# Performance work log

Hardware: AMD Instinct MI355X
Metric: run time of the kernel (lower is better)

## Reference

```python
import jax, jax.numpy as jnp
import numpy as np

N_HEAD = 8
HIDDEN = 512
HEAD_DIM = HIDDEN // N_HEAD
EPS = 1e-5


def _layernorm(x, g, b):
    mu = jnp.mean(x, axis=-1, keepdims=True)
    var = jnp.var(x, axis=-1, keepdims=True)
    return (x - mu) * jax.lax.rsqrt(var + EPS) * g + b


def setup_inputs() -> dict:
    key = jax.random.key(0)
    ks = jax.random.split(key, 12)
    s = 1.0 / np.sqrt(HIDDEN)
    x = jax.random.normal(ks[0], (4, 2048, HIDDEN), dtype=jnp.float32)
    # per-head Q/K/V projections stacked: [H, D, dh] weights, [H, dh] biases
    Wq = jax.random.uniform(ks[1], (N_HEAD, HIDDEN, HEAD_DIM), minval=-s, maxval=s, dtype=jnp.float32)
    bq = jax.random.uniform(ks[2], (N_HEAD, HEAD_DIM), minval=-s, maxval=s, dtype=jnp.float32)
    Wk = jax.random.uniform(ks[3], (N_HEAD, HIDDEN, HEAD_DIM), minval=-s, maxval=s, dtype=jnp.float32)
    bk = jax.random.uniform(ks[4], (N_HEAD, HEAD_DIM), minval=-s, maxval=s, dtype=jnp.float32)
    Wv = jax.random.uniform(ks[5], (N_HEAD, HIDDEN, HEAD_DIM), minval=-s, maxval=s, dtype=jnp.float32)
    bv = jax.random.uniform(ks[6], (N_HEAD, HEAD_DIM), minval=-s, maxval=s, dtype=jnp.float32)
    Wm = jax.random.uniform(ks[7], (HIDDEN, HIDDEN), minval=-s, maxval=s, dtype=jnp.float32)
    bm = jax.random.uniform(ks[8], (HIDDEN,), minval=-s, maxval=s, dtype=jnp.float32)
    Wo = jax.random.uniform(ks[9], (HIDDEN, HIDDEN), minval=-s, maxval=s, dtype=jnp.float32)
    bo = jax.random.uniform(ks[10], (HIDDEN,), minval=-s, maxval=s, dtype=jnp.float32)
    g1 = jnp.ones((HIDDEN,), jnp.float32); b1 = jnp.zeros((HIDDEN,), jnp.float32)
    g2 = jnp.ones((HIDDEN,), jnp.float32); b2 = jnp.zeros((HIDDEN,), jnp.float32)
    return {"x": x, "g1": g1, "b1": b1, "Wq": Wq, "bq": bq, "Wk": Wk, "bk": bk,
            "Wv": Wv, "bv": bv, "Wm": Wm, "bm": bm, "g2": g2, "b2": b2, "Wo": Wo, "bo": bo}


def reference(x, g1, b1, Wq, bq, Wk, bk, Wv, bv, Wm, bm, g2, b2, Wo, bo):
    h = _layernorm(x, g1, b1)                                 # [B,S,D]
    # stacked per-head projections: [B,H,S,dh]
    q = jnp.einsum('bsd,hde->bhse', h, Wq) + bq[None, :, None, :]
    k = jnp.einsum('bsd,hde->bhse', h, Wk) + bk[None, :, None, :]
    v = jnp.einsum('bsd,hde->bhse', h, Wv) + bv[None, :, None, :]
    scores = jnp.einsum('bhse,bhte->bhst', q, k) / jnp.sqrt(jnp.float32(HEAD_DIM))
    attn = jax.nn.softmax(scores, axis=-1)                    # [B,H,S,S]
    out = jnp.einsum('bhst,bhte->bhse', attn, v)              # [B,H,S,dh]
    B, H, S, E = out.shape
    out_mha = jnp.transpose(out, (0, 2, 1, 3)).reshape(B, S, H * E)  # concat heads
    h_ln_post = out_mha @ Wm + bm + x
    h_fc = _layernorm(h_ln_post, g2, b2)
    return jax.nn.relu(h_fc @ Wo + bo) + h_ln_post
```

## Files before the change

### kernel.cpp

```cpp
#include <hip/hip_runtime.h>
#include <hip/hip_bf16.h>


typedef __attribute__((ext_vector_type(8))) short bf16x8;
typedef __attribute__((ext_vector_type(4))) float f32x4;
typedef __attribute__((ext_vector_type(16))) float f32x16;
typedef __attribute__((ext_vector_type(8))) unsigned short u16x8;

typedef union { bf16x8 v; unsigned u[4]; u16x8 s; } frag_u;

typedef const unsigned int __attribute__((address_space(1)))* gas_t;
typedef unsigned int __attribute__((address_space(3)))* las_t;
static __device__ __forceinline__ void glds16(const void* g, void* l) {
    __builtin_amdgcn_global_load_lds((gas_t)g, (las_t)l, 16, 0, 0);
}

static __device__ __forceinline__ unsigned short f2b(float f) {
    union { float f; unsigned u; } a; a.f = f;
    unsigned r = a.u + 0x7FFFu + ((a.u >> 16) & 1u);
    return (unsigned short)(r >> 16);
}
static __device__ __forceinline__ float b2f(unsigned short u) {
    union { unsigned u; float f; } c; c.u = ((unsigned)u) << 16; return c.f;
}
static __device__ __forceinline__ unsigned pack_bf16(float lo, float hi) {
    __hip_bfloat162 p = __float22bfloat162_rn(make_float2(lo, hi));
    unsigned r; __builtin_memcpy(&r, &p, 4); return r;
}
static __device__ __forceinline__ float fexp2(float x) {
#if __has_builtin(__builtin_amdgcn_exp2f)
    return __builtin_amdgcn_exp2f(x);
#else
    return exp2f(x);
#endif
}
static __device__ __forceinline__ void swap32(int hi, unsigned a, unsigned b,
                                              unsigned& x, unsigned& y) {
#if __has_builtin(__builtin_amdgcn_permlane32_swap)
    typedef __attribute__((ext_vector_type(2))) int i32x2;
    i32x2 r = __builtin_amdgcn_permlane32_swap((int)a, (int)b, false, false);
    x = (unsigned)r[0]; y = (unsigned)r[1];
#else
    unsigned ta = (unsigned)__shfl_xor((int)a, 32);
    unsigned tb = (unsigned)__shfl_xor((int)b, 32);
    x = hi ? tb : a;
    y = hi ? b : ta;
#endif
}

static __device__ __forceinline__ void ln_row(
    const float* __restrict__ X, const float* __restrict__ gam,
    const float* __restrict__ bet, unsigned short* __restrict__ O,
    int row, int lane)
{
    const float4* xr = (const float4*)(X + (size_t)row * 512);
    float4 v0 = xr[lane * 2], v1 = xr[lane * 2 + 1];
    float vv[8] = {v0.x, v0.y, v0.z, v0.w, v1.x, v1.y, v1.z, v1.w};
    float s = 0.f, s2 = 0.f;
    #pragma unroll
    for (int j = 0; j < 8; ++j) { s += vv[j]; s2 += vv[j] * vv[j]; }
    #pragma unroll
    for (int d = 1; d < 64; d <<= 1) { s += __shfl_xor(s, d); s2 += __shfl_xor(s2, d); }
    float mean = s * (1.0f / 512.0f);
    float var  = s2 * (1.0f / 512.0f) - mean * mean;
    float rstd = rsqrtf(var + 1e-5f);
    int c = lane * 8;
    u16x8 o;
    #pragma unroll
    for (int j = 0; j < 8; ++j) o[j] = f2b((vv[j] - mean) * rstd * gam[c + j] + bet[c + j]);
    *(u16x8*)(O + (size_t)row * 512 + c) = o;
}

__global__ __launch_bounds__(256) void prep_ln_k(
    const float* __restrict__ Wq, const float* __restrict__ Wk, const float* __restrict__ Wv,
    const float* __restrict__ Wm, const float* __restrict__ Wo,
    unsigned short* __restrict__ wqT, unsigned short* __restrict__ wkT,
    unsigned short* __restrict__ wvT, unsigned short* __restrict__ wmT,
    unsigned short* __restrict__ woT,
    const float* __restrict__ X, const float* __restrict__ g1,
    const float* __restrict__ b1, unsigned short* __restrict__ h1)
{
    int bx = blockIdx.x;
    if (bx < 1024) {
        int idx = bx * 256 + threadIdx.x;
        int n = idx >> 9, k = idx & 511;
        int h = n >> 6, e = n & 63;
        size_t src_qkv = ((size_t)h * 512 + k) * 64 + e;
        wqT[idx] = f2b(Wq[src_qkv]);
        wkT[idx] = f2b(Wk[src_qkv]);
        wvT[idx] = f2b(Wv[src_qkv]);
        wmT[idx] = f2b(Wm[(size_t)k * 512 + n]);
        woT[idx] = f2b(Wo[(size_t)k * 512 + n]);
    } else {
        int row = (bx - 1024) * 4 + (threadIdx.x >> 6);
        ln_row(X, g1, b1, h1, row, threadIdx.x & 63);
    }
}

__global__ __launch_bounds__(256) void ln4_k(
    const float* __restrict__ X, const float* __restrict__ gam,
    const float* __restrict__ bet, unsigned short* __restrict__ O)
{
    int row = blockIdx.x * 4 + (threadIdx.x >> 6);
    ln_row(X, gam, bet, O, row, threadIdx.x & 63);
}

__global__ __launch_bounds__(256) void gemm_qkv_k(
    const unsigned short* __restrict__ A, const unsigned short* __restrict__ Bt,
    const float* __restrict__ bq, const float* __restrict__ bk, const float* __restrict__ bv,
    unsigned short* __restrict__ Qo, unsigned short* __restrict__ Ko,
    unsigned short* __restrict__ VtO)
{
    __shared__ unsigned short Al[2][128 * 32];
    __shared__ unsigned short Bl[2][128 * 32];
    int tid = threadIdx.x;
    int wid = tid >> 6, lane = tid & 63;
    int lr = lane & 15, lg = lane >> 4;
    int m0 = blockIdx.x * 128, n0 = blockIdx.y * 128;
    int seg = blockIdx.y >> 2;
    int wr = (wid >> 1) * 64, wc = (wid & 1) * 64;
    f32x4 acc[4][4] = {};
    const unsigned short* Ag = A  + (size_t)(m0 + wid * 32 + (lane >> 2)) * 512 + (lane & 3) * 8;
    const unsigned short* Bg = Bt + (size_t)(n0 + wid * 32 + (lane >> 2)) * 512 + (lane & 3) * 8;
    const int lofs = wid * 32 * 32;

    auto STAGE = [&](int buf, int k0) {
        glds16(Ag + k0,            Al[buf] + lofs);
        glds16(Ag + k0 + 16 * 512, Al[buf] + lofs + 16 * 32);
        glds16(Bg + k0,            Bl[buf] + lofs);
        glds16(Bg + k0 + 16 * 512, Bl[buf] + lofs + 16 * 32);
    };
    auto COMPUTE = [&](int buf) {
        bf16x8 af[4], bfr[4];
        #pragma unroll
        for (int m = 0; m < 4; ++m) af[m]  = *(const bf16x8*)(Al[buf] + (wr + m * 16 + lr) * 32 + lg * 8);
        #pragma unroll
        for (int n = 0; n < 4; ++n) bfr[n] = *(const bf16x8*)(Bl[buf] + (wc + n * 16 + lr) * 32 + lg * 8);
        #pragma unroll
        for (int m = 0; m < 4; ++m)
            #pragma unroll
            for (int n = 0; n < 4; ++n)
                acc[m][n] = __builtin_amdgcn_mfma_f32_16x16x32_bf16(af[m], bfr[n], acc[m][n], 0, 0, 0);
    };

    STAGE(0, 0);
    #pragma unroll 1
    for (int k0 = 0; k0 < 512; k0 += 64) {
        __syncthreads();
        if (k0 + 32 < 512) STAGE(1, k0 + 32);
        COMPUTE(0);
        __syncthreads();
        if (k0 + 64 < 512) STAGE(0, k0 + 64);
        COMPUTE(1);
    }

    const float* bb = seg == 0 ? bq : (seg == 1 ? bk : bv);
    unsigned short* dst = seg == 0 ? Qo : Ko;
    #pragma unroll
    for (int m = 0; m < 4; ++m)
      #pragma unroll
      for (int n = 0; n < 4; ++n) {
        int gr0 = m0 + wr + m * 16 + 4 * lg;
        int nc  = ((blockIdx.y & 3) << 7) + wc + n * 16 + lr;
        float bias = bb[nc];
        if (seg < 2) {
            #pragma unroll
            for (int j = 0; j < 4; ++j)
                dst[(size_t)(gr0 + j) * 512 + nc] = f2b(acc[m][n][j] + bias);
        } else {
            int bbk = gr0 >> 11, ss = gr0 & 2047, hh = nc >> 6, ee = nc & 63;
            ushort4 pv;
            pv.x = f2b(acc[m][n][0] + bias);
            pv.y = f2b(acc[m][n][1] + bias);
            pv.z = f2b(acc[m][n][2] + bias);
            pv.w = f2b(acc[m][n][3] + bias);
            *(ushort4*)&VtO[((size_t)((bbk * 8 + hh) * 64 + ee) << 11) + ss] = pv;
        }
      }
}

template<int MODE>
__global__ __launch_bounds__(256) void gemm_n64_k(
    const unsigned short* __restrict__ A, const unsigned short* __restrict__ Bt,
    const float* __restrict__ bias, const float* __restrict__ aux,
    float* __restrict__ Cout)
{
    __shared__ unsigned short Al[2][128 * 32];
    __shared__ unsigned short Bl[2][64 * 32];
    int tid = threadIdx.x;
    int wid = tid >> 6, lane = tid & 63;
    int lr = lane & 15, lg = lane >> 4;
    int m0 = blockIdx.x * 128, n0 = blockIdx.y * 64;
    int wr = wid * 32;
    f32x4 acc[2][4] = {};
    const unsigned short* Ag = A  + (size_t)(m0 + wid * 32 + (lane >> 2)) * 512 + (lane & 3) * 8;
    const unsigned short* Bg = Bt + (size_t)(n0 + wid * 16 + (lane >> 2)) * 512 + (lane & 3) * 8;
    const int aofs = wid * 32 * 32;
    const int bofs = wid * 16 * 32;

    auto STAGE = [&](int buf, int k0) {
        glds16(Ag + k0,            Al[buf] + aofs);
        glds16(Ag + k0 + 16 * 512, Al[buf] + aofs + 16 * 32);
        glds16(Bg + k0,            Bl[buf] + bofs);
    };
    auto COMPUTE = [&](int buf) {
        bf16x8 af[2], bfr[4];
        #pragma unroll
        for (int m = 0; m < 2; ++m) af[m]  = *(const bf16x8*)(Al[buf] + (wr + m * 16 + lr) * 32 + lg * 8);
        #pragma unroll
        for (int n = 0; n < 4; ++n) bfr[n] = *(const bf16x8*)(Bl[buf] + (n * 16 + lr) * 32 + lg * 8);
        #pragma unroll
        for (int m = 0; m < 2; ++m)
            #pragma unroll
            for (int n = 0; n < 4; ++n)
                acc[m][n] = __builtin_amdgcn_mfma_f32_16x16x32_bf16(af[m], bfr[n], acc[m][n], 0, 0, 0);
    };

    STAGE(0, 0);
    #pragma unroll 1
    for (int k0 = 0; k0 < 512; k0 += 64) {
        __syncthreads();
        if (k0 + 32 < 512) STAGE(1, k0 + 32);
        COMPUTE(0);
        __syncthreads();
        if (k0 + 64 < 512) STAGE(0, k0 + 64);
        COMPUTE(1);
    }

    #pragma unroll
    for (int m = 0; m < 2; ++m)
      #pragma unroll
      for (int n = 0; n < 4; ++n)
        #pragma unroll
        for (int j = 0; j < 4; ++j) {
            int gr = m0 + wr + m * 16 + 4 * lg + j;
            int gc = n0 + n * 16 + lr;
            float v = acc[m][n][j] + bias[gc];
            if (MODE == 3) v = v > 0.0f ? v : 0.0f;
            Cout[(size_t)gr * 512 + gc] = v + aux[(size_t)gr * 512 + gc];
        }
}

__global__ __launch_bounds__(128) void attn12_k(
    const unsigned short* __restrict__ Q, const unsigned short* __restrict__ K,
    const unsigned short* __restrict__ Vt, unsigned short* __restrict__ O)
{
    __shared__ __align__(16) unsigned short KlA[4096], KlB[4096];
    __shared__ __align__(16) unsigned short VlA[4096], VlB[4096];

    const int tid  = threadIdx.x;
    const int lane = tid & 63;
    const int q31  = lane & 31;
    const int hi   = lane >> 5;
    const int wid  = tid >> 6;

    int bid = blockIdx.x;
    int xcd = bid & 7, idx = bid >> 3;
    int bh  = xcd + 8 * (idx >> 5);
    int qt  = idx & 31;
    int b = bh >> 3, h = bh & 7;
    int q0 = qt * 64 + wid * 32;

    const unsigned short* Qb = Q  + (size_t)b * 2048 * 512 + h * 64;
    const unsigned short* Kb = K  + (size_t)b * 2048 * 512 + h * 64;
    const unsigned short* Vb = Vt + (size_t)(b * 8 + h) * 64 * 2048;

    frag_u qf[4];
    const float qs = 0.125f * 1.44269504f;
    #pragma unroll
    for (int ds = 0; ds < 4; ++ds) {
        u16x8 raw = *(const u16x8*)(Qb + (size_t)(q0 + q31) * 512 + ds * 16 + hi * 8);
        #pragma unroll
        for (int i = 0; i < 4; ++i)
            qf[ds].u[i] = pack_bf16(b2f(raw[2 * i]) * qs, b2f(raw[2 * i + 1]) * qs);
    }

    frag_u onesf;
    #pragma unroll
    for (int i = 0; i < 4; ++i) onesf.u[i] = 0x3F803F80u;

    unsigned soff[8];
    #pragma unroll
    for (int j = 0; j < 8; ++j) {
        int row31 = j * 4 + (lane >> 4);
        int x = (lane & 15) ^ (row31 & 15);
        int t = 32 * (x >> 3) + row31;
        int s = x & 7;
        soff[j] = (wid == 0) ? (unsigned)(t * 512 + s * 8)
                             : (unsigned)(t * 2048 + s * 8);
    }
    const unsigned short* Gb = (wid == 0) ? Kb : Vb;

    auto STAGE = [&](unsigned short* buf, int t0) {
        const unsigned short* g = Gb + (wid == 0 ? (size_t)t0 * 512 : (size_t)t0);
        #pragma unroll
        for (int j = 0; j < 8; ++j)
            glds16(g + soff[j], buf + j * 512);
    };

    f32x16 acc0, acc1, lacc;
    #pragma unroll
    for (int r = 0; r < 16; ++r) { acc0[r] = 0.0f; acc1[r] = 0.0f; lacc[r] = 0.0f; }
    const int swz = (q31 & 15) << 4;

    auto COMPUTE = [&](const unsigned short* Kh_, const unsigned short* Vh_) {
        const char* Kh = (const char*)Kh_;
        const char* Vh = (const char*)Vh_;
        f32x16 s0, s1;
        #pragma unroll
        for (int r = 0; r < 16; ++r) { s0[r] = 0.0f; s1[r] = 0.0f; }
        __builtin_amdgcn_s_setprio(1);
        #pragma unroll
        for (int ds = 0; ds < 4; ++ds) {
            bf16x8 k0 = *(const bf16x8*)(Kh + q31 * 256 + ((ds * 32 + hi * 16) ^ swz));
            bf16x8 k1 = *(const bf16x8*)(Kh + q31 * 256 + ((128 + ds * 32 + hi * 16) ^ swz));
            s0 = __builtin_amdgcn_mfma_f32_32x32x16_bf16(k0, qf[ds].v, s0, 0, 0, 0);
            s1 = __builtin_amdgcn_mfma_f32_32x32x16_bf16(k1, qf[ds].v, s1, 0, 0, 0);
        }
        __builtin_amdgcn_s_setprio(0);

        #pragma unroll
        for (int r = 0; r < 16; ++r) {
            s0[r] = fexp2(s0[r]);
            s1[r] = fexp2(s1[r]);
        }

        frag_u pa[4];
        #pragma unroll
        for (int g = 0; g < 2; ++g) {
            unsigned A0 = pack_bf16(s0[8 * g + 0], s0[8 * g + 1]);
            unsigned A1 = pack_bf16(s0[8 * g + 2], s0[8 * g + 3]);
            unsigned A2 = pack_bf16(s0[8 * g + 4], s0[8 * g + 5]);
            unsigned A3 = pack_bf16(s0[8 * g + 6], s0[8 * g + 7]);
            swap32(hi, A0, A2, pa[g].u[0], pa[g].u[2]);
            swap32(hi, A1, A3, pa[g].u[1], pa[g].u[3]);
            unsigned B0 = pack_bf16(s1[8 * g + 0], s1[8 * g + 1]);
            unsigned B1 = pack_bf16(s1[8 * g + 2], s1[8 * g + 3]);
            unsigned B2 = pack_bf16(s1[8 * g + 4], s1[8 * g + 5]);
            unsigned B3 = pack_bf16(s1[8 * g + 6], s1[8 * g + 7]);
            swap32(hi, B0, B2, pa[2 + g].u[0], pa[2 + g].u[2]);
            swap32(hi, B1, B3, pa[2 + g].u[1], pa[2 + g].u[3]);
        }

        __builtin_amdgcn_s_setprio(1);
        #pragma unroll
        for (int ks = 0; ks < 4; ++ks) {
            bf16x8 v0 = *(const bf16x8*)(Vh + q31 * 256 + ((ks * 32 + hi * 16) ^ swz));
            bf16x8 v1 = *(const bf16x8*)(Vh + q31 * 256 + ((128 + ks * 32 + hi * 16) ^ swz));
            acc0 = __builtin_amdgcn_mfma_f32_32x32x16_bf16(pa[ks].v, v0, acc0, 0, 0, 0);
            acc1 = __builtin_amdgcn_mfma_f32_32x32x16_bf16(pa[ks].v, v1, acc1, 0, 0, 0);
            lacc = __builtin_amdgcn_mfma_f32_32x32x16_bf16(pa[ks].v, onesf.v, lacc, 0, 0, 0);
        }
        __builtin_amdgcn_s_setprio(0);
    };

    STAGE(wid == 0 ? KlA : VlA, 0);
    __syncthreads();

    #pragma unroll 1
    for (int it = 0; it < 32; it += 2) {
        if (it + 1 < 32) STAGE(wid == 0 ? KlB : VlB, (it + 1) * 64);
        COMPUTE(KlA, VlA);
        __syncthreads();
        if (it + 2 < 32) STAGE(wid == 0 ? KlA : VlA, (it + 2) * 64);
        COMPUTE(KlB, VlB);
        __syncthreads();
    }

    #pragma unroll
    for (int r = 0; r < 16; ++r) {
        int cr = (r & 3) + 8 * (r >> 2) + 4 * hi;
        float li = 1.0f / lacc[r];
        size_t rowoff = (size_t)(b * 2048 + q0 + cr) * 512 + h * 64 + q31;
        O[rowoff]      = f2b(acc0[r] * li);
        O[rowoff + 32] = f2b(acc1[r] * li);
    }
}

extern "C" void kernel_launch(void* const* d_in, const int* in_sizes, int n_in,
                              void* d_out, int out_size, void* d_ws, size_t ws_size,
                              hipStream_t stream)
{
    const float* x  = (const float*)d_in[0];
    const float* g1 = (const float*)d_in[1];
    const float* b1 = (const float*)d_in[2];
    const float* Wq = (const float*)d_in[3];
    const float* bq = (const float*)d_in[4];
    const float* Wk = (const float*)d_in[5];
    const float* bk = (const float*)d_in[6];
    const float* Wv = (const float*)d_in[7];
    const float* bv = (const float*)d_in[8];
    const float* Wm = (const float*)d_in[9];
    const float* bm = (const float*)d_in[10];
    const float* g2 = (const float*)d_in[11];
    const float* b2 = (const float*)d_in[12];
    const float* Wo = (const float*)d_in[13];
    const float* bo = (const float*)d_in[14];
    float* out = (float*)d_out;

    char* ws = (char*)d_ws;
    const size_t EB = (size_t)8192 * 512 * 2;
    unsigned short* h1  = (unsigned short*)(ws);
    unsigned short* qb  = (unsigned short*)(ws + EB);
    unsigned short* kb  = (unsigned short*)(ws + 2 * EB);
    unsigned short* vtb = (unsigned short*)(ws + 3 * EB);
    unsigned short* ao  = (unsigned short*)(ws + 4 * EB);
    unsigned short* h2  = (unsigned short*)(ws + 5 * EB);
    float*          hlp = (float*)(ws + 6 * EB);
    unsigned short* wqT = (unsigned short*)(ws + 8 * EB);
    unsigned short* wkT = wqT + 512 * 512;
    unsigned short* wvT = wkT + 512 * 512;
    unsigned short* wmT = wvT + 512 * 512;
    unsigned short* woT = wmT + 512 * 512;

    prep_ln_k<<<3072, 256, 0, stream>>>(Wq, Wk, Wv, Wm, Wo,
                                        wqT, wkT, wvT, wmT, woT,
                                        x, g1, b1, h1);
    gemm_qkv_k<<<dim3(64, 12), 256, 0, stream>>>(h1, wqT, bq, bk, bv, qb, kb, vtb);
    attn12_k<<<1024, 128, 0, stream>>>(qb, kb, vtb, ao);
    gemm_n64_k<2><<<dim3(64, 8), 256, 0, stream>>>(ao, wmT, bm, x, hlp);
    ln4_k<<<2048, 256, 0, stream>>>(hlp, g2, b2, h2);
    gemm_n64_k<3><<<dim3(64, 8), 256, 0, stream>>>(h2, woT, bo, hlp, out);
}
```

Baseline: 130.7 us.

## Software-pipeline attention loop so next tile's QK overlaps current softmax and PV

The attention loop is split into a QK stage and a softmax+PV stage. The QK scores for tile t+1 are now computed while tile t goes through exp, packing and the PV MFMAs. K and V staging are separated so each K tile is loaded one step earlier than its V tile. The goal is to hide the exp/pack VALU work and the LDS latency behind MFMA work. In exchange, a second set of score accumulators stays live, which raises VGPR pressure and can lower occupancy.

```diff
diff --git a/kernel.cpp b/kernel.cpp
--- a/kernel.cpp
+++ b/kernel.cpp
@@ -241,7 +241,7 @@
         }
 }
 
-__global__ __launch_bounds__(128) void attn12_k(
+__global__ __launch_bounds__(128) void attn14_k(
     const unsigned short* __restrict__ Q, const unsigned short* __restrict__ K,
     const unsigned short* __restrict__ Vt, unsigned short* __restrict__ O)
 {
@@ -289,13 +289,20 @@
         soff[j] = (wid == 0) ? (unsigned)(t * 512 + s * 8)
                              : (unsigned)(t * 2048 + s * 8);
     }
-    const unsigned short* Gb = (wid == 0) ? Kb : Vb;
-
-    auto STAGE = [&](unsigned short* buf, int t0) {
-        const unsigned short* g = Gb + (wid == 0 ? (size_t)t0 * 512 : (size_t)t0);
-        #pragma unroll
-        for (int j = 0; j < 8; ++j)
-            glds16(g + soff[j], buf + j * 512);
+
+    auto STAGE_K = [&](unsigned short* buf, int tok0) {
+        if (wid == 0) {
+            const unsigned short* g = Kb + (size_t)tok0 * 512;
+            #pragma unroll
+            for (int j = 0; j < 8; ++j) glds16(g + soff[j], buf + j * 512);
+        }
+    };
+    auto STAGE_V = [&](unsigned short* buf, int tok0) {
+        if (wid == 1) {
+            const unsigned short* g = Vb + tok0;
+            #pragma unroll
+            for (int j = 0; j < 8; ++j) glds16(g + soff[j], buf + j * 512);
+        }
     };
 
     f32x16 acc0, acc1, lacc;
@@ -303,13 +310,10 @@
     for (int r = 0; r < 16; ++r) { acc0[r] = 0.0f; acc1[r] = 0.0f; lacc[r] = 0.0f; }
     const int swz = (q31 & 15) << 4;
 
-    auto COMPUTE = [&](const unsigned short* Kh_, const unsigned short* Vh_) {
+    auto QK = [&](const unsigned short* Kh_, f32x16& s0, f32x16& s1) {
         const char* Kh = (const char*)Kh_;
-        const char* Vh = (const char*)Vh_;
-        f32x16 s0, s1;
         #pragma unroll
         for (int r = 0; r < 16; ++r) { s0[r] = 0.0f; s1[r] = 0.0f; }
-        __builtin_amdgcn_s_setprio(1);
         #pragma unroll
         for (int ds = 0; ds < 4; ++ds) {
             bf16x8 k0 = *(const bf16x8*)(Kh + q31 * 256 + ((ds * 32 + hi * 16) ^ swz));
@@ -317,14 +321,15 @@
             s0 = __builtin_amdgcn_mfma_f32_32x32x16_bf16(k0, qf[ds].v, s0, 0, 0, 0);
             s1 = __builtin_amdgcn_mfma_f32_32x32x16_bf16(k1, qf[ds].v, s1, 0, 0, 0);
         }
-        __builtin_amdgcn_s_setprio(0);
-
+    };
+
+    auto SMPV = [&](f32x16& s0, f32x16& s1, const unsigned short* Vh_) {
+        const char* Vh = (const char*)Vh_;
         #pragma unroll
         for (int r = 0; r < 16; ++r) {
             s0[r] = fexp2(s0[r]);
             s1[r] = fexp2(s1[r]);
         }
-
         frag_u pa[4];
         #pragma unroll
         for (int g = 0; g < 2; ++g) {
@@ -341,7 +346,6 @@
             swap32(hi, B0, B2, pa[2 + g].u[0], pa[2 + g].u[2]);
             swap32(hi, B1, B3, pa[2 + g].u[1], pa[2 + g].u[3]);
         }
-
         __builtin_amdgcn_s_setprio(1);
         #pragma unroll
         for (int ks = 0; ks < 4; ++ks) {
@@ -354,16 +358,28 @@
         __builtin_amdgcn_s_setprio(0);
     };
 
-    STAGE(wid == 0 ? KlA : VlA, 0);
+    f32x16 p0, p1, n0, n1;
+
+    STAGE_K(KlA, 0);
+    STAGE_V(VlA, 0);
     __syncthreads();
+    STAGE_K(KlB, 64);
+    QK(KlA, p0, p1);
+    __syncthreads();
 
     #pragma unroll 1
-    for (int it = 0; it < 32; it += 2) {
-        if (it + 1 < 32) STAGE(wid == 0 ? KlB : VlB, (it + 1) * 64);
-        COMPUTE(KlA, VlA);
-        __syncthreads();
-        if (it + 2 < 32) STAGE(wid == 0 ? KlA : VlA, (it + 2) * 64);
-        COMPUTE(KlB, VlB);
+    for (int t = 0; t < 32; t += 2) {
+        if (t + 2 < 32) STAGE_K(KlA, (t + 2) * 64);
+        STAGE_V(VlB, (t + 1) * 64);
+        QK(KlB, n0, n1);
+        SMPV(p0, p1, VlA);
+        __syncthreads();
+        if (t + 3 < 32) STAGE_K(KlB, (t + 3) * 64);
+        if (t + 2 < 32) {
+            STAGE_V(VlA, (t + 2) * 64);
+            QK(KlA, p0, p1);
+        }
+        SMPV(n0, n1, VlB);
         __syncthreads();
     }
 
@@ -417,7 +433,7 @@
                                         wqT, wkT, wvT, wmT, woT,
                                         x, g1, b1, h1);
     gemm_qkv_k<<<dim3(64, 12), 256, 0, stream>>>(h1, wqT, bq, bk, bv, qb, kb, vtb);
-    attn12_k<<<1024, 128, 0, stream>>>(qb, kb, vtb, ao);
+    attn14_k<<<1024, 128, 0, stream>>>(qb, kb, vtb, ao);
     gemm_n64_k<2><<<dim3(64, 8), 256, 0, stream>>>(ao, wmT, bm, x, hlp);
     ln4_k<<<2048, 256, 0, stream>>>(hlp, g2, b2, h2);
     gemm_n64_k<3><<<dim3(64, 8), 256, 0, stream>>>(h2, woT, bo, hlp, out);
```

Result: slower. 140.0 us (+7.2%).
